# Optimization experiments

Hardware: AMD Instinct MI355X
Metric: run time of the kernel (lower is better)

Reference implementation:

```python
import jax, jax.numpy as jnp
import numpy as np

B, S, D, H = 4, 2048, 1024, 16
HD = D // H  # head_dim = 64


def setup_inputs() -> dict:
    key = jax.random.key(0)
    k1, k2, k3, k4, k5 = jax.random.split(key, 5)
    x = jax.random.normal(k1, (B, S, D), dtype=jnp.float32)
    # per-head QKV projection weights (H separate Linear(D, 3*HD) layers, batched)
    Wqkv = jax.random.normal(k2, (H, D, 3 * HD), dtype=jnp.float32) * (D ** -0.5)
    bqkv = jax.random.normal(k3, (H, 3 * HD), dtype=jnp.float32) * 0.02
    # output projection Linear(D, D)
    Wo = jax.random.normal(k4, (D, D), dtype=jnp.float32) * (D ** -0.5)
    bo = jax.random.normal(k5, (D,), dtype=jnp.float32) * 0.02
    return {"x": x, "Wqkv": Wqkv, "bqkv": bqkv, "Wo": Wo, "bo": bo}


def reference(x, Wqkv, bqkv, Wo, bo):
    # Batched per-head QKV projection: [B,S,D] x [H,D,3*HD] -> [B,H,S,3*HD]
    qkv = jnp.einsum('bsd,hde->bhse', x, Wqkv) + bqkv[None, :, None, :]
    q, k, v = jnp.split(qkv, 3, axis=-1)  # each [B,H,S,HD]
    scale = HD ** -0.5
    scores = jnp.einsum('bhqe,bhke->bhqk', q, k) * scale  # [B,H,S,S]
    causal = jnp.tril(jnp.ones((S, S), dtype=bool))
    scores = jnp.where(causal, scores, -jnp.inf)
    attn = jax.nn.softmax(scores, axis=-1)
    # dropout is identity in eval mode
    out = jnp.einsum('bhqk,bhke->bhqe', attn, v)  # [B,H,S,HD]
    out = jnp.transpose(out, (0, 2, 1, 3)).reshape(B, S, D)  # concat heads
    return out @ Wo + bo
```

## Files before the change

### kernel.cpp

```cpp
#include <hip/hip_runtime.h>
#include <hip/hip_bf16.h>

#define B_ 4
#define S_ 2048
#define D_ 1024
#define H_ 16
#define HD_ 64
#define M_TOK 8192
#define QSCALE 0.18033688f

typedef __attribute__((ext_vector_type(4))) float f32x4;
typedef __attribute__((ext_vector_type(8))) short short8;
typedef __attribute__((ext_vector_type(4))) short short4_t;

__device__ inline short f2bf(float f) {
  unsigned u = __builtin_bit_cast(unsigned, f);
  u += 0x7fff + ((u >> 16) & 1);
  return (short)(u >> 16);
}
__device__ inline short f2bf_trunc(float f) {
  return (short)(__builtin_bit_cast(unsigned, f) >> 16);
}

typedef __attribute__((address_space(1))) const unsigned int gas_u32;
typedef __attribute__((address_space(3))) unsigned int las_u32;
__device__ inline void gload_lds16(const void* g, void* l) {
  __builtin_amdgcn_global_load_lds((gas_u32*)g, (las_u32*)l, 16, 0, 0);
}

__global__ __launch_bounds__(256) void conv_x_kernel(
    const float* __restrict__ x, short* __restrict__ xb) {
  size_t base = ((size_t)blockIdx.x * 256 + threadIdx.x) * 8;
  f32x4 v0 = *reinterpret_cast<const f32x4*>(&x[base]);
  f32x4 v1 = *reinterpret_cast<const f32x4*>(&x[base + 4]);
  short8 o;
  o[0]=f2bf(v0[0]); o[1]=f2bf(v0[1]); o[2]=f2bf(v0[2]); o[3]=f2bf(v0[3]);
  o[4]=f2bf(v1[0]); o[5]=f2bf(v1[1]); o[6]=f2bf(v1[2]); o[7]=f2bf(v1[3]);
  *reinterpret_cast<short8*>(&xb[base]) = o;
}

__global__ __launch_bounds__(256) void conv_wqkv_kernel(
    const float* __restrict__ Wqkv, short* __restrict__ wqkvt) {
  const int h = blockIdx.x;
  const int k0 = blockIdx.y * 32;
  const int tid = threadIdx.x;
  __shared__ short T[192 * 40];
#pragma unroll
  for (int i = 0; i < 6; ++i) {
    int iv = tid + i * 256;
    int k = iv / 48;
    int e4 = (iv % 48) * 4;
    f32x4 v = *reinterpret_cast<const f32x4*>(&Wqkv[((size_t)h * D_ + k0 + k) * 192 + e4]);
#pragma unroll
    for (int j = 0; j < 4; ++j) T[(e4 + j) * 40 + k] = f2bf(v[j]);
  }
  __syncthreads();
#pragma unroll
  for (int i = 0; i < 6; ++i) {
    int iv = tid + i * 256;
    int e = iv >> 3;
    int g4 = iv & 7;
    short4_t o = *reinterpret_cast<const short4_t*>(&T[e * 40 + g4 * 4]);
    *reinterpret_cast<short4_t*>(&wqkvt[(size_t)(h * 192 + e) * 1024 + k0 + g4 * 4]) = o;
  }
}

__global__ __launch_bounds__(256) void conv_wo_kernel(
    const float* __restrict__ Wo, short* __restrict__ wot) {
  const int k0 = blockIdx.x * 32;
  const int n0 = blockIdx.y * 128;
  const int tid = threadIdx.x;
  __shared__ short T[128 * 40];
#pragma unroll
  for (int i = 0; i < 4; ++i) {
    int iv = tid + i * 256;
    int k = iv >> 5;
    int n4 = (iv & 31) * 4;
    f32x4 v = *reinterpret_cast<const f32x4*>(&Wo[(size_t)(k0 + k) * 1024 + n0 + n4]);
#pragma unroll
    for (int j = 0; j < 4; ++j) T[(n4 + j) * 40 + k] = f2bf(v[j]);
  }
  __syncthreads();
#pragma unroll
  for (int i = 0; i < 4; ++i) {
    int iv = tid + i * 256;
    int e = iv >> 3;
    int g4 = iv & 7;
    short4_t o = *reinterpret_cast<const short4_t*>(&T[e * 40 + g4 * 4]);
    *reinterpret_cast<short4_t*>(&wot[(size_t)(n0 + e) * 1024 + k0 + g4 * 4]) = o;
  }
}

template<int EPI>
__global__ __launch_bounds__(256, 3) void gemm3_kernel(
    const short* __restrict__ A, const short* __restrict__ Bt,
    const float* __restrict__ bias,
    short* __restrict__ qb, short* __restrict__ kb, short* __restrict__ vt,
    float* __restrict__ out) {
  constexpr int KD = 1024;
  constexpr int NKT = KD / 32;
  const int m0 = blockIdx.x * 128;
  const int n0 = blockIdx.y * 128;
  const int tid = threadIdx.x;
  const int lane = tid & 63, wv = tid >> 6;
  const int wr = wv >> 1, wc = wv & 1;
  const int g = lane >> 4, c = lane & 15;

  __shared__ short lds_pool[24576];

  const f32x4 zero4 = {0.f, 0.f, 0.f, 0.f};
  f32x4 acc[4][4];
#pragma unroll
  for (int i = 0; i < 4; ++i)
#pragma unroll
    for (int j = 0; j < 4; ++j) acc[i][j] = zero4;

  auto STAGE = [&](int kt, int buf) {
    const short* asrc = A + (size_t)m0 * KD + kt * 32;
#pragma unroll
    for (int i = 0; i < 2; ++i) {
      int ch = tid + i * 256;
      int row = ch >> 2;
      int slot = (ch & 3) ^ ((row >> 1) & 3);
      gload_lds16(asrc + (size_t)row * KD + slot * 8,
                  &lds_pool[buf * 4096 + ch * 8]);
    }
    const short* bsrc = Bt + (size_t)n0 * KD + kt * 32;
#pragma unroll
    for (int i = 0; i < 2; ++i) {
      int ch = tid + i * 256;
      int row = ch >> 2;
      int slot = (ch & 3) ^ ((row >> 1) & 3);
      gload_lds16(bsrc + (size_t)row * KD + slot * 8,
                  &lds_pool[12288 + buf * 4096 + ch * 8]);
    }
  };

  STAGE(0, 0);
  STAGE(1, 1);
  int cb = 0;

  const int sread = (g ^ ((c >> 1) & 3)) * 8;

  for (int t = 0; t < NKT; ++t) {
    __builtin_amdgcn_sched_barrier(0);
    __builtin_amdgcn_s_barrier();
    __builtin_amdgcn_sched_barrier(0);
    if (t + 2 < NKT) {
      int sb = (cb + 2 >= 3) ? cb - 1 : cb + 2;
      STAGE(t + 2, sb);
      asm volatile("s_waitcnt vmcnt(8)" ::: "memory");
    } else if (t + 1 < NKT) {
      asm volatile("s_waitcnt vmcnt(4)" ::: "memory");
    } else {
      asm volatile("s_waitcnt vmcnt(0)" ::: "memory");
    }
    __builtin_amdgcn_s_barrier();
    __builtin_amdgcn_sched_barrier(0);

    const short* Ab = &lds_pool[cb * 4096];
    const short* Bb = &lds_pool[12288 + cb * 4096];
    short8 a[4], b[4];
#pragma unroll
    for (int mt = 0; mt < 4; ++mt)
      a[mt] = *reinterpret_cast<const short8*>(&Ab[(wr * 64 + mt * 16 + c) * 32 + sread]);
#pragma unroll
    for (int nt = 0; nt < 4; ++nt)
      b[nt] = *reinterpret_cast<const short8*>(&Bb[(wc * 64 + nt * 16 + c) * 32 + sread]);
    __builtin_amdgcn_s_setprio(1);
#pragma unroll
    for (int mt = 0; mt < 4; ++mt)
#pragma unroll
      for (int nt = 0; nt < 4; ++nt)
        acc[mt][nt] = __builtin_amdgcn_mfma_f32_16x16x32_bf16(a[mt], b[nt], acc[mt][nt], 0, 0, 0);
    __builtin_amdgcn_s_setprio(0);
    cb = (cb + 1 == 3) ? 0 : cb + 1;
  }

#pragma unroll
  for (int mt = 0; mt < 4; ++mt) {
#pragma unroll
    for (int nt = 0; nt < 4; ++nt) {
      int n = n0 + wc * 64 + nt * 16 + c;
      float bv = bias[n];
      int m_base = m0 + wr * 64 + mt * 16 + g * 4;
      if (EPI == 0) {
        int h = n / 192, e = n % 192;
        int bb2 = m_base >> 11, s0 = m_base & 2047;
        size_t plane = (size_t)(bb2 * H_ + h) * (S_ * HD_);
        if (e < 64) {
          size_t bp = plane + (size_t)(s0 >> 4) * 1024 + (e >> 3) * 128 + (s0 & 15) * 8 + (e & 7);
#pragma unroll
          for (int r = 0; r < 4; ++r)
            qb[bp + r * 8] = f2bf((acc[mt][nt][r] + bv) * QSCALE);
        } else if (e < 128) {
          int ek = e - 64;
          size_t bp = plane + (size_t)(s0 >> 4) * 1024 + (ek >> 3) * 128 + (s0 & 15) * 8 + (ek & 7);
#pragma unroll
          for (int r = 0; r < 4; ++r)
            kb[bp + r * 8] = f2bf(acc[mt][nt][r] + bv);
        } else {
          int hd = e - 128;
          size_t bp = plane + (size_t)((hd >> 4) * 64 + (s0 >> 5)) * 512 +
                      ((s0 >> 3) & 3) * 128 + (hd & 15) * 8 + (s0 & 7);
          short4_t vv;
#pragma unroll
          for (int r = 0; r < 4; ++r) vv[r] = f2bf(acc[mt][nt][r] + bv);
          *reinterpret_cast<short4_t*>(&vt[bp]) = vv;
        }
      } else {
#pragma unroll
        for (int r = 0; r < 4; ++r)
          out[(size_t)(m_base + r) * D_ + n] = acc[mt][nt][r] + bv;
      }
    }
  }
}

struct KF32 { short8 f[4]; };

__device__ __forceinline__ void load_kf32(KF32& k, const short* __restrict__ kbh,
                                          int ktb, int lane) {
#pragma unroll
  for (int cc = 0; cc < 2; ++cc)
#pragma unroll
    for (int t = 0; t < 2; ++t)
      k.f[cc * 2 + t] = *reinterpret_cast<const short8*>(
          &kbh[(size_t)(ktb * 2 + t) * 1024 + cc * 512 + lane * 8]);
}

__global__ __launch_bounds__(256, 3) void attn_kernel(
    const short* __restrict__ qb, const short* __restrict__ kb,
    const short* __restrict__ vt, short* __restrict__ av) {
  const int orig = blockIdx.x;
  const int xcd = orig & 7;
  const int local = orig >> 3;
  const int bh = xcd * 8 + (local & 7);
  const int qt = 15 - (local >> 3);
  const int bb = bh >> 4, h = bh & 15;
  const int tid = threadIdx.x;
  const int lane = tid & 63, wv = tid >> 6;
  const int g = lane >> 4, c = lane & 15;
  const int q0 = qt * 128;
  const int r0 = q0 + wv * 32;

  __shared__ short Ps[4][32 * 40];
  short* Pw = Ps[wv];

  const short* qbh = qb + (size_t)bh * S_ * HD_;
  const short* kbh = kb + (size_t)bh * S_ * HD_;
  const short* vth = vt + (size_t)bh * HD_ * S_;

  short8 ones;
#pragma unroll
  for (int j = 0; j < 8; ++j) ones[j] = (short)0x3F80;

  const f32x4 zero4 = {0.f, 0.f, 0.f, 0.f};

  short8 qf[2][2];
#pragma unroll
  for (int mt = 0; mt < 2; ++mt)
#pragma unroll
    for (int cc = 0; cc < 2; ++cc)
      qf[mt][cc] = *reinterpret_cast<const short8*>(
          &qbh[(size_t)(r0 / 16 + mt) * 1024 + cc * 512 + lane * 8]);

  f32x4 acc_o[2][4];
  f32x4 lacc[2];
#pragma unroll
  for (int mt = 0; mt < 2; ++mt) {
    lacc[mt] = zero4;
#pragma unroll
    for (int nt = 0; nt < 4; ++nt) acc_o[mt][nt] = zero4;
  }

  const int diag = 4 * qt + wv;
  const int nk = diag + 1;

  KF32 kA, kB;
  load_kf32(kA, kbh, 0, lane);

  auto body = [&](int ktb, KF32& kc, KF32& kn) {
    const int k0 = ktb * 32;
    short8 vf[4];
#pragma unroll
    for (int nt = 0; nt < 4; ++nt)
      vf[nt] = *reinterpret_cast<const short8*>(
          &vth[(size_t)(nt * 64 + ktb) * 512 + lane * 8]);
    f32x4 sc[2][2];
#pragma unroll
    for (int mt = 0; mt < 2; ++mt)
#pragma unroll
      for (int t = 0; t < 2; ++t) sc[mt][t] = zero4;
#pragma unroll
    for (int cc = 0; cc < 2; ++cc)
#pragma unroll
      for (int mt = 0; mt < 2; ++mt)
#pragma unroll
        for (int t = 0; t < 2; ++t)
          sc[mt][t] = __builtin_amdgcn_mfma_f32_16x16x32_bf16(
              qf[mt][cc], kc.f[cc * 2 + t], sc[mt][t], 0, 0, 0);
    int ktbn = ktb + 1;
    if (ktbn >= S_ / 32) ktbn = 0;
    load_kf32(kn, kbh, ktbn, lane);
    if (ktb == diag) {
#pragma unroll
      for (int mt = 0; mt < 2; ++mt)
#pragma unroll
        for (int t = 0; t < 2; ++t) {
          const int key = k0 + t * 16 + c;
#pragma unroll
          for (int r = 0; r < 4; ++r) {
            const int qi = r0 + mt * 16 + g * 4 + r;
            if (key > qi) sc[mt][t][r] = -INFINITY;
          }
        }
    }
#pragma unroll
    for (int mt = 0; mt < 2; ++mt)
#pragma unroll
      for (int t = 0; t < 2; ++t)
#pragma unroll
        for (int r = 0; r < 4; ++r) {
          float pf = __builtin_exp2f(sc[mt][t][r]);
          Pw[(mt * 16 + g * 4 + r) * 40 + t * 16 + c] = f2bf_trunc(pf);
        }
    short8 pa[2];
#pragma unroll
    for (int mt = 0; mt < 2; ++mt)
      pa[mt] = *reinterpret_cast<const short8*>(&Pw[(mt * 16 + c) * 40 + g * 8]);
#pragma unroll
    for (int mt = 0; mt < 2; ++mt)
      lacc[mt] = __builtin_amdgcn_mfma_f32_16x16x32_bf16(pa[mt], ones, lacc[mt], 0, 0, 0);
#pragma unroll
    for (int mt = 0; mt < 2; ++mt)
#pragma unroll
      for (int nt = 0; nt < 4; ++nt)
        acc_o[mt][nt] = __builtin_amdgcn_mfma_f32_16x16x32_bf16(
            pa[mt], vf[nt], acc_o[mt][nt], 0, 0, 0);
  };

  int ktb = 0;
  for (; ktb + 1 < nk; ktb += 2) {
    body(ktb,     kA, kB);
    body(ktb + 1, kB, kA);
  }
  if (ktb < nk) body(ktb, kA, kB);

#pragma unroll
  for (int mt = 0; mt < 2; ++mt) {
    float inv[4];
#pragma unroll
    for (int r = 0; r < 4; ++r) inv[r] = 1.0f / lacc[mt][r];
#pragma unroll
    for (int nt = 0; nt < 4; ++nt)
#pragma unroll
      for (int r = 0; r < 4; ++r) {
        int R = r0 + mt * 16 + g * 4 + r;
        av[(size_t)(bb * S_ + R) * D_ + h * HD_ + nt * 16 + c] =
            f2bf(acc_o[mt][nt][r] * inv[r]);
      }
  }
}

extern "C" void kernel_launch(void* const* d_in, const int* in_sizes, int n_in,
                              void* d_out, int out_size, void* d_ws, size_t ws_size,
                              hipStream_t stream) {
  const float* x    = (const float*)d_in[0];
  const float* Wqkv = (const float*)d_in[1];
  const float* bqkv = (const float*)d_in[2];
  const float* Wo   = (const float*)d_in[3];
  const float* bo   = (const float*)d_in[4];
  float* out = (float*)d_out;

  const size_t NTOK = (size_t)B_ * H_ * S_ * HD_;
  short* xb    = (short*)d_ws;
  short* wqkvt = xb + (size_t)M_TOK * D_;
  short* wot   = wqkvt + (size_t)3072 * 1024;
  short* qb    = wot + (size_t)1024 * 1024;
  short* kb    = qb + NTOK;
  short* vt    = kb + NTOK;
  short* av    = xb;

  conv_x_kernel   <<<4096, 256, 0, stream>>>(x, xb);
  conv_wqkv_kernel<<<dim3(16, 32), 256, 0, stream>>>(Wqkv, wqkvt);
  conv_wo_kernel  <<<dim3(32, 8), 256, 0, stream>>>(Wo, wot);
  gemm3_kernel<0> <<<dim3(64, 24), 256, 0, stream>>>(xb, wqkvt, bqkv, qb, kb, vt, nullptr);
  attn_kernel     <<<1024, 256, 0, stream>>>(qb, kb, vt, av);
  gemm3_kernel<1> <<<dim3(64, 8), 256, 0, stream>>>(av, wot, bo, nullptr, nullptr, nullptr, out);
}
```

Baseline: 168.0 us.

## Pre-pack weights into MFMA fragment layout and load B directly to registers

The weight conversion kernels now write Wqkv and Wo in a packed per-16-column-tile layout that matches the MFMA B-operand fragment order. The GEMM then loads B fragments straight from global memory into registers, double-buffered, rather than staging them through LDS. A is staged through a 4-deep LDS ring with a manually unrolled schedule. The attention kernel's launch bounds are also raised to 4 blocks per CU. This cuts LDS traffic and footprint in the GEMMs, at the cost of exposing global-load latency on the B operand and adding register pressure.

```diff
diff --git a/kernel.cpp b/kernel.cpp
--- a/kernel.cpp
+++ b/kernel.cpp
@@ -27,6 +27,7 @@
 __device__ inline void gload_lds16(const void* g, void* l) {
   __builtin_amdgcn_global_load_lds((gas_u32*)g, (las_u32*)l, 16, 0, 0);
 }
+
 
 __global__ __launch_bounds__(256) void conv_x_kernel(
     const float* __restrict__ x, short* __restrict__ xb) {
@@ -40,7 +41,7 @@
 }
 
 __global__ __launch_bounds__(256) void conv_wqkv_kernel(
-    const float* __restrict__ Wqkv, short* __restrict__ wqkvt) {
+    const float* __restrict__ Wqkv, short* __restrict__ wp) {
   const int h = blockIdx.x;
   const int k0 = blockIdx.y * 32;
   const int tid = threadIdx.x;
@@ -56,17 +57,20 @@
   }
   __syncthreads();
 #pragma unroll
-  for (int i = 0; i < 6; ++i) {
-    int iv = tid + i * 256;
-    int e = iv >> 3;
-    int g4 = iv & 7;
-    short4_t o = *reinterpret_cast<const short4_t*>(&T[e * 40 + g4 * 4]);
-    *reinterpret_cast<short4_t*>(&wqkvt[(size_t)(h * 192 + e) * 1024 + k0 + g4 * 4]) = o;
+  for (int i = 0; i < 3; ++i) {
+    int u = tid + i * 256;
+    int e16 = u >> 6;
+    int rem = u & 63;
+    int e = e16 * 16 + (rem & 15);
+    int k8 = (rem >> 4) * 8;
+    short8 o = *reinterpret_cast<const short8*>(&T[e * 40 + k8]);
+    *reinterpret_cast<short8*>(
+        &wp[(size_t)(h * 12 + e16) * 16384 + blockIdx.y * 512 + rem * 8]) = o;
   }
 }
 
 __global__ __launch_bounds__(256) void conv_wo_kernel(
-    const float* __restrict__ Wo, short* __restrict__ wot) {
+    const float* __restrict__ Wo, short* __restrict__ wp) {
   const int k0 = blockIdx.x * 32;
   const int n0 = blockIdx.y * 128;
   const int tid = threadIdx.x;
@@ -82,18 +86,20 @@
   }
   __syncthreads();
 #pragma unroll
-  for (int i = 0; i < 4; ++i) {
-    int iv = tid + i * 256;
-    int e = iv >> 3;
-    int g4 = iv & 7;
-    short4_t o = *reinterpret_cast<const short4_t*>(&T[e * 40 + g4 * 4]);
-    *reinterpret_cast<short4_t*>(&wot[(size_t)(n0 + e) * 1024 + k0 + g4 * 4]) = o;
+  for (int i = 0; i < 2; ++i) {
+    int u = tid + i * 256;
+    int ntile = u >> 6;
+    int rem = u & 63;
+    short8 o = *reinterpret_cast<const short8*>(
+        &T[(ntile * 16 + (rem & 15)) * 40 + (rem >> 4) * 8]);
+    *reinterpret_cast<short8*>(
+        &wp[(size_t)((n0 >> 4) + ntile) * 16384 + blockIdx.x * 512 + rem * 8]) = o;
   }
 }
 
 template<int EPI>
-__global__ __launch_bounds__(256, 3) void gemm3_kernel(
-    const short* __restrict__ A, const short* __restrict__ Bt,
+__global__ __launch_bounds__(256, 3) void gemm4_kernel(
+    const short* __restrict__ A, const short* __restrict__ Bp,
     const float* __restrict__ bias,
     short* __restrict__ qb, short* __restrict__ kb, short* __restrict__ vt,
     float* __restrict__ out) {
@@ -106,7 +112,7 @@
   const int wr = wv >> 1, wc = wv & 1;
   const int g = lane >> 4, c = lane & 15;
 
-  __shared__ short lds_pool[24576];
+  __shared__ short As[4 * 4096];
 
   const f32x4 zero4 = {0.f, 0.f, 0.f, 0.f};
   f32x4 acc[4][4];
@@ -115,6 +121,14 @@
 #pragma unroll
     for (int j = 0; j < 4; ++j) acc[i][j] = zero4;
 
+  const short* bbase = Bp + (size_t)((n0 + wc * 64) >> 4) * 16384 + lane * 8;
+  short8 bb0[4], bb1[4];
+
+  auto LOADB = [&](int t, short8* br) {
+#pragma unroll
+    for (int nt = 0; nt < 4; ++nt)
+      br[nt] = *reinterpret_cast<const short8*>(&bbase[(size_t)nt * 16384 + t * 512]);
+  };
   auto STAGE = [&](int kt, int buf) {
     const short* asrc = A + (size_t)m0 * KD + kt * 32;
 #pragma unroll
@@ -122,60 +136,45 @@
       int ch = tid + i * 256;
       int row = ch >> 2;
       int slot = (ch & 3) ^ ((row >> 1) & 3);
-      gload_lds16(asrc + (size_t)row * KD + slot * 8,
-                  &lds_pool[buf * 4096 + ch * 8]);
-    }
-    const short* bsrc = Bt + (size_t)n0 * KD + kt * 32;
-#pragma unroll
-    for (int i = 0; i < 2; ++i) {
-      int ch = tid + i * 256;
-      int row = ch >> 2;
-      int slot = (ch & 3) ^ ((row >> 1) & 3);
-      gload_lds16(bsrc + (size_t)row * KD + slot * 8,
-                  &lds_pool[12288 + buf * 4096 + ch * 8]);
+      gload_lds16(asrc + (size_t)row * KD + slot * 8, &As[buf * 4096 + ch * 8]);
     }
   };
-
-  STAGE(0, 0);
-  STAGE(1, 1);
-  int cb = 0;
-
   const int sread = (g ^ ((c >> 1) & 3)) * 8;
-
-  for (int t = 0; t < NKT; ++t) {
-    __builtin_amdgcn_sched_barrier(0);
-    __builtin_amdgcn_s_barrier();
-    __builtin_amdgcn_sched_barrier(0);
-    if (t + 2 < NKT) {
-      int sb = (cb + 2 >= 3) ? cb - 1 : cb + 2;
-      STAGE(t + 2, sb);
-      asm volatile("s_waitcnt vmcnt(8)" ::: "memory");
-    } else if (t + 1 < NKT) {
-      asm volatile("s_waitcnt vmcnt(4)" ::: "memory");
-    } else {
-      asm volatile("s_waitcnt vmcnt(0)" ::: "memory");
-    }
-    __builtin_amdgcn_s_barrier();
-    __builtin_amdgcn_sched_barrier(0);
-
-    const short* Ab = &lds_pool[cb * 4096];
-    const short* Bb = &lds_pool[12288 + cb * 4096];
-    short8 a[4], b[4];
+  auto COMP = [&](int buf, short8* br) {
+    const short* Ab = &As[buf * 4096];
+    short8 a[4];
 #pragma unroll
     for (int mt = 0; mt < 4; ++mt)
       a[mt] = *reinterpret_cast<const short8*>(&Ab[(wr * 64 + mt * 16 + c) * 32 + sread]);
-#pragma unroll
-    for (int nt = 0; nt < 4; ++nt)
-      b[nt] = *reinterpret_cast<const short8*>(&Bb[(wc * 64 + nt * 16 + c) * 32 + sread]);
     __builtin_amdgcn_s_setprio(1);
 #pragma unroll
     for (int mt = 0; mt < 4; ++mt)
 #pragma unroll
       for (int nt = 0; nt < 4; ++nt)
-        acc[mt][nt] = __builtin_amdgcn_mfma_f32_16x16x32_bf16(a[mt], b[nt], acc[mt][nt], 0, 0, 0);
+        acc[mt][nt] = __builtin_amdgcn_mfma_f32_16x16x32_bf16(a[mt], br[nt], acc[mt][nt], 0, 0, 0);
     __builtin_amdgcn_s_setprio(0);
-    cb = (cb + 1 == 3) ? 0 : cb + 1;
-  }
+  };
+
+#define BAR1 __builtin_amdgcn_sched_barrier(0); __builtin_amdgcn_s_barrier(); __builtin_amdgcn_sched_barrier(0)
+#define VMW(N) asm volatile("s_waitcnt vmcnt(" #N ")" ::: "memory")
+
+  STAGE(0, 0); STAGE(1, 1); LOADB(0, bb0);
+
+#pragma unroll 1
+  for (int p = 0; p < 7; ++p) {
+    const int tb = p * 4;
+    BAR1; STAGE(tb + 2, 2); LOADB(tb + 1, bb1); VMW(6); BAR1; COMP(0, bb0);
+    BAR1; STAGE(tb + 3, 3); LOADB(tb + 2, bb0); VMW(6); BAR1; COMP(1, bb1);
+    BAR1; STAGE(tb + 4, 0); LOADB(tb + 3, bb1); VMW(6); BAR1; COMP(2, bb0);
+    BAR1; STAGE(tb + 5, 1); LOADB(tb + 4, bb0); VMW(6); BAR1; COMP(3, bb1);
+  }
+  BAR1; STAGE(30, 2); LOADB(29, bb1); VMW(6); BAR1; COMP(0, bb0);
+  BAR1; STAGE(31, 3); LOADB(30, bb0); VMW(6); BAR1; COMP(1, bb1);
+  BAR1;               LOADB(31, bb1); VMW(4); BAR1; COMP(2, bb0);
+  BAR1;                               VMW(0); BAR1; COMP(3, bb1);
+
+#undef BAR1
+#undef VMW
 
 #pragma unroll
   for (int mt = 0; mt < 4; ++mt) {
@@ -229,7 +228,7 @@
           &kbh[(size_t)(ktb * 2 + t) * 1024 + cc * 512 + lane * 8]);
 }
 
-__global__ __launch_bounds__(256, 3) void attn_kernel(
+__global__ __launch_bounds__(256, 4) void attn_kernel(
     const short* __restrict__ qb, const short* __restrict__ kb,
     const short* __restrict__ vt, short* __restrict__ av) {
   const int orig = blockIdx.x;
@@ -385,7 +384,7 @@
   conv_x_kernel   <<<4096, 256, 0, stream>>>(x, xb);
   conv_wqkv_kernel<<<dim3(16, 32), 256, 0, stream>>>(Wqkv, wqkvt);
   conv_wo_kernel  <<<dim3(32, 8), 256, 0, stream>>>(Wo, wot);
-  gemm3_kernel<0> <<<dim3(64, 24), 256, 0, stream>>>(xb, wqkvt, bqkv, qb, kb, vt, nullptr);
+  gemm4_kernel<0> <<<dim3(64, 24), 256, 0, stream>>>(xb, wqkvt, bqkv, qb, kb, vt, nullptr);
   attn_kernel     <<<1024, 256, 0, stream>>>(qb, kb, vt, av);
-  gemm3_kernel<1> <<<dim3(64, 8), 256, 0, stream>>>(av, wot, bo, nullptr, nullptr, nullptr, out);
-}
+  gemm4_kernel<1> <<<dim3(64, 8), 256, 0, stream>>>(av, wot, bo, nullptr, nullptr, nullptr, out);
+}
```

Result: no change. 165.9 us (-1.2%).
